# Optimization experiments

Measured on AMD Instinct MI355X. Metric: run time of the kernel, lower is better.

The kernel has to match this reference:

```python
import jax, jax.numpy as jnp
import numpy as np

B, C, IN, OUT = 2048, 64, 512, 512


def setup_inputs() -> dict:
    key = jax.random.key(0)
    k1, k2, k3 = jax.random.split(key, 3)
    x = jax.random.normal(k1, (B, IN), dtype=jnp.float32)
    index = jax.random.randint(k2, (B,), 0, C, dtype=jnp.int64)
    # kaiming_uniform-ish init: bound = sqrt(6 / ((1 + 5) * fan_in)) = 1/sqrt(fan_in)
    bound = 1.0 / np.sqrt(IN)
    weight = jax.random.uniform(k3, (C, OUT, IN), dtype=jnp.float32,
                                minval=-bound, maxval=bound)
    return {"input": x, "index": index, "weight": weight}


def reference(input, index, weight):
    # weight: (C, OUT, IN); index: (B,); input: (B, IN)
    w = weight[index]                      # (B, OUT, IN) gathered per-sample matrix
    return jnp.einsum('boi,bi->bo', w, input)  # batched matvec -> (B, OUT)
```

## Files before the change

### kernel.cpp

```cpp
#include <hip/hip_runtime.h>


constexpr int Bsz  = 2048;
constexpr int Ccnt = 64;
constexpr int INF  = 512;
constexpr int OUTF = 512;
constexpr int THREADS = 256;
constexpr int OT  = 16;
constexpr int TPB = 4;
constexpr int NBLK = Ccnt * (OUTF / (OT * TPB));

typedef __attribute__((ext_vector_type(8))) short bf16x8;
typedef __attribute__((ext_vector_type(4))) float f32x4;

#if __has_builtin(__builtin_amdgcn_cvt_pk_bf16_f32)
typedef __attribute__((ext_vector_type(2))) __bf16 bf16x2_t;
__device__ __forceinline__ int cvt2i(float a, float b) {
    union { bf16x2_t v; int i; } u;
    u.v = __builtin_amdgcn_cvt_pk_bf16_f32(a, b);
    return u.i;
}
#else
__device__ __forceinline__ unsigned f2bf(float f) {
    union { float f; unsigned u; } v; v.f = f;
    return (v.u + 0x7FFFu + ((v.u >> 16) & 1u)) >> 16;
}
__device__ __forceinline__ int cvt2i(float a, float b) {
    return (int)(f2bf(a) | (f2bf(b) << 16));
}
#endif

__device__ __forceinline__ bf16x8 cvt8(float4 a, float4 b) {
    union { bf16x8 v; int i[4]; } u;
    u.i[0] = cvt2i(a.x, a.y);
    u.i[1] = cvt2i(a.z, a.w);
    u.i[2] = cvt2i(b.x, b.y);
    u.i[3] = cvt2i(b.z, b.w);
    return u.v;
}

__device__ __forceinline__ void gld_lds16(const float* g, float* l) {
    __builtin_amdgcn_global_load_lds(
        (const __attribute__((address_space(1))) float*)g,
        (__attribute__((address_space(3))) float*)l, 16, 0, 0);
}

__device__ __forceinline__ void barrier_lgkm() {
    asm volatile("s_waitcnt lgkmcnt(0)" ::: "memory");
    __builtin_amdgcn_s_barrier();
    asm volatile("" ::: "memory");
}

__device__ __forceinline__ void stage_tile(const float* wt, float* dst,
                                           int wave, int lane) {
#pragma unroll
    for (int i = 0; i < 8; ++i) {
        const int inst = wave * 8 + i;
        const int r = inst >> 1;
        const int h = inst & 1;
        const int p = r & 7;
        const float* src = wt + (size_t)r * INF + (h * 64 + (lane ^ p)) * 4;
        gld_lds16(src, dst + inst * 256);
    }
}

__global__ __launch_bounds__(THREADS, 2)
void switching_linear_kernel(const float* __restrict__ x,
                             const int* __restrict__ idx,
                             const float* __restrict__ w,
                             float* __restrict__ out) {
    __shared__ float Wl[2][OT * INF];
    __shared__ unsigned short list[Bsz];
    __shared__ int ls_n;
    __shared__ float red[2][3][4][64];

    const int tid  = threadIdx.x;
    const int wave = tid >> 6;
    const int lane = tid & 63;

    const int bid   = ((int)blockIdx.x & 7) * (NBLK / 8) + ((int)blockIdx.x >> 3);
    const int c     = bid >> 3;
    const int obase = (bid & 7) * (OT * TPB);

    if (tid == 0) ls_n = 0;
    __syncthreads();

    const float* wc = w + (size_t)c * OUTF * INF + (size_t)obase * INF;

    stage_tile(wc, Wl[0], wave, lane);

    int my[8];
#pragma unroll
    for (int i = 0; i < 8; ++i) my[i] = idx[tid + i * THREADS];
#pragma unroll
    for (int i = 0; i < 8; ++i)
        if (my[i] == c) list[atomicAdd(&ls_n, 1)] = (unsigned short)(tid + i * THREADS);

    const int mrow = lane & 15;
    const int quad = lane >> 4;
    const int k0   = wave * (INF / 4);
    const int p    = mrow & 7;

    int n = 0;

    for (int ot = 0; ot < TPB; ++ot) {
        __syncthreads();
        if (ot == 0) {
            n = ls_n;
            if (n == 0) return;
        }
        if (ot + 1 < TPB)
            stage_tile(wc + (size_t)((ot + 1) * OT) * INF, Wl[(ot + 1) & 1],
                       wave, lane);

        const float* Wb = Wl[ot & 1];
        const int o0 = obase + ot * OT;

        bf16x8 wf[4];
#pragma unroll
        for (int t = 0; t < 4; ++t) {
            const int gb = (k0 >> 2) + t * 8 + quad * 2;
            float4 a0 = *(const float4*)&Wb[mrow * INF + ((gb)     ^ p) * 4];
            float4 a1 = *(const float4*)&Wb[mrow * INF + ((gb + 1) ^ p) * 4];
            wf[t] = cvt8(a0, a1);
        }

        for (int s0 = 0; s0 < n; s0 += 64) {
            const int rem = n - s0;
            const int ng  = rem >= 64 ? 4 : (rem + 15) >> 4;

            f32x4 acc[4];
#pragma unroll
            for (int g = 0; g < 4; ++g) acc[g] = (f32x4){0.f, 0.f, 0.f, 0.f};

#pragma unroll
            for (int g = 0; g < 4; ++g) {
                if (g < ng) {
                    const int s  = s0 + g * 16 + mrow;
                    const int sc = s < n ? s : n - 1;
                    const float* bp = x + (size_t)list[sc] * INF + k0 + quad * 8;
#pragma unroll
                    for (int i = 0; i < 4; ++i) {
                        float4 b0 = *(const float4*)(bp + i * 32);
                        float4 b1 = *(const float4*)(bp + i * 32 + 4);
                        acc[g] = __builtin_amdgcn_mfma_f32_16x16x32_bf16(
                                     wf[i], cvt8(b0, b1), acc[g], 0, 0, 0);
                    }
                }
            }

#pragma unroll
            for (int r0 = 0; r0 < 4; r0 += 2) {
                if (r0 < ng) {
                    if (wave != 0) {
#pragma unroll
                        for (int g = 0; g < 2; ++g) {
                            if (r0 + g < ng) {
#pragma unroll
                                for (int j = 0; j < 4; ++j)
                                    red[g][wave - 1][j][lane] = acc[r0 + g][j];
                            }
                        }
                    }
                    barrier_lgkm();
                    if (wave == 0) {
#pragma unroll
                        for (int g = 0; g < 2; ++g) {
                            if (r0 + g < ng) {
                                const int s = s0 + (r0 + g) * 16 + mrow;
                                if (s < n) {
                                    f32x4 a = acc[r0 + g];
#pragma unroll
                                    for (int wv2 = 0; wv2 < 3; ++wv2)
#pragma unroll
                                        for (int j = 0; j < 4; ++j)
                                            a[j] += red[g][wv2][j][lane];
                                    float* dst = out + (size_t)list[s] * OUTF
                                                     + o0 + quad * 4;
                                    *(float4*)dst = make_float4(a[0], a[1],
                                                                a[2], a[3]);
                                }
                            }
                        }
                    }
                    barrier_lgkm();
                }
            }
        }
    }
}

extern "C" void kernel_launch(void* const* d_in, const int* in_sizes, int n_in,
                              void* d_out, int out_size, void* d_ws, size_t ws_size,
                              hipStream_t stream) {
    const float* x   = (const float*)d_in[0];
    const int*   idx = (const int*)d_in[1];
    const float* w   = (const float*)d_in[2];
    float* out = (float*)d_out;

    switching_linear_kernel<<<dim3(NBLK), dim3(THREADS), 0, stream>>>(x, idx, w, out);
}
```

Before: 116.1 us.

## Split samples across waves instead of K, drop cross-wave LDS reduction

Each wave now owns a 16-sample group and covers the full K=512 dimension, so the cross-wave LDS reduction and its barriers are removed. The gathered x rows are loaded once into registers, converted to bf16, and reused across all four output tiles. Weight tiles are prefetched two ahead with vmcnt-based waits. The cost is higher register pressure (a 32-float4 raw buffer plus 16 bf16x8 fragments). With n around 32 per class, some waves sit idle, and each wave now reads more LDS per MFMA.

Result: faster. 106.4 us (-8.3%).

```diff
diff --git a/kernel.cpp b/kernel.cpp
--- a/kernel.cpp
+++ b/kernel.cpp
@@ -8,6 +8,7 @@
 constexpr int THREADS = 256;
 constexpr int OT  = 16;
 constexpr int TPB = 4;
+constexpr int NBUF = 2;
 constexpr int NBLK = Ccnt * (OUTF / (OT * TPB));
 
 typedef __attribute__((ext_vector_type(8))) short bf16x8;
@@ -51,6 +52,19 @@
     asm volatile("" ::: "memory");
 }
 
+__device__ __forceinline__ void vm8_barrier() {
+    asm volatile("s_waitcnt vmcnt(8)" ::: "memory");
+    __builtin_amdgcn_sched_barrier(0);
+    __builtin_amdgcn_s_barrier();
+    asm volatile("" ::: "memory");
+}
+__device__ __forceinline__ void vm0_barrier() {
+    asm volatile("s_waitcnt vmcnt(0)" ::: "memory");
+    __builtin_amdgcn_sched_barrier(0);
+    __builtin_amdgcn_s_barrier();
+    asm volatile("" ::: "memory");
+}
+
 __device__ __forceinline__ void stage_tile(const float* wt, float* dst,
                                            int wave, int lane) {
 #pragma unroll
@@ -69,10 +83,9 @@
                              const int* __restrict__ idx,
                              const float* __restrict__ w,
                              float* __restrict__ out) {
-    __shared__ float Wl[2][OT * INF];
+    __shared__ float Wl[NBUF][OT * INF];
     __shared__ unsigned short list[Bsz];
     __shared__ int ls_n;
-    __shared__ float red[2][3][4][64];
 
     const int tid  = threadIdx.x;
     const int wave = tid >> 6;
@@ -85,10 +98,6 @@
     if (tid == 0) ls_n = 0;
     __syncthreads();
 
-    const float* wc = w + (size_t)c * OUTF * INF + (size_t)obase * INF;
-
-    stage_tile(wc, Wl[0], wave, lane);
-
     int my[8];
 #pragma unroll
     for (int i = 0; i < 8; ++i) my[i] = idx[tid + i * THREADS];
@@ -96,96 +105,97 @@
     for (int i = 0; i < 8; ++i)
         if (my[i] == c) list[atomicAdd(&ls_n, 1)] = (unsigned short)(tid + i * THREADS);
 
+    __syncthreads();
+    const int n = ls_n;
+    if (n == 0) return;
+
     const int mrow = lane & 15;
     const int quad = lane >> 4;
-    const int k0   = wave * (INF / 4);
     const int p    = mrow & 7;
-
-    int n = 0;
+    const float* wc = w + (size_t)c * OUTF * INF + (size_t)obase * INF;
+
+    const int ng0    = (n >= 64) ? 4 : ((n + 15) >> 4);
+    const bool active = (wave < ng0);
+    const int s_my   = wave * 16 + mrow;
+    const int sc     = s_my < n ? s_my : n - 1;
+
+    float4 raw[32];
+    if (active) {
+        const float* bp = x + (size_t)list[sc] * INF + quad * 8;
+#pragma unroll
+        for (int kk = 0; kk < 16; ++kk) {
+            raw[2 * kk]     = *(const float4*)(bp + kk * 32);
+            raw[2 * kk + 1] = *(const float4*)(bp + kk * 32 + 4);
+        }
+    }
+    __builtin_amdgcn_sched_barrier(0);
+
+    stage_tile(wc,                    Wl[0], wave, lane);
+    stage_tile(wc + (size_t)OT * INF, Wl[1], wave, lane);
+
+    asm volatile("s_waitcnt vmcnt(16)" ::: "memory");
+    __builtin_amdgcn_sched_barrier(0);
+
+    bf16x8 xf[16];
+    if (active) {
+#pragma unroll
+        for (int kk = 0; kk < 16; ++kk)
+            xf[kk] = cvt8(raw[2 * kk], raw[2 * kk + 1]);
+    }
+
+    vm8_barrier();
 
     for (int ot = 0; ot < TPB; ++ot) {
-        __syncthreads();
-        if (ot == 0) {
-            n = ls_n;
-            if (n == 0) return;
-        }
-        if (ot + 1 < TPB)
-            stage_tile(wc + (size_t)((ot + 1) * OT) * INF, Wl[(ot + 1) & 1],
-                       wave, lane);
-
         const float* Wb = Wl[ot & 1];
         const int o0 = obase + ot * OT;
 
-        bf16x8 wf[4];
-#pragma unroll
-        for (int t = 0; t < 4; ++t) {
-            const int gb = (k0 >> 2) + t * 8 + quad * 2;
-            float4 a0 = *(const float4*)&Wb[mrow * INF + ((gb)     ^ p) * 4];
-            float4 a1 = *(const float4*)&Wb[mrow * INF + ((gb + 1) ^ p) * 4];
-            wf[t] = cvt8(a0, a1);
-        }
-
-        for (int s0 = 0; s0 < n; s0 += 64) {
-            const int rem = n - s0;
-            const int ng  = rem >= 64 ? 4 : (rem + 15) >> 4;
-
-            f32x4 acc[4];
-#pragma unroll
-            for (int g = 0; g < 4; ++g) acc[g] = (f32x4){0.f, 0.f, 0.f, 0.f};
-
-#pragma unroll
-            for (int g = 0; g < 4; ++g) {
-                if (g < ng) {
-                    const int s  = s0 + g * 16 + mrow;
-                    const int sc = s < n ? s : n - 1;
-                    const float* bp = x + (size_t)list[sc] * INF + k0 + quad * 8;
-#pragma unroll
-                    for (int i = 0; i < 4; ++i) {
-                        float4 b0 = *(const float4*)(bp + i * 32);
-                        float4 b1 = *(const float4*)(bp + i * 32 + 4);
-                        acc[g] = __builtin_amdgcn_mfma_f32_16x16x32_bf16(
-                                     wf[i], cvt8(b0, b1), acc[g], 0, 0, 0);
-                    }
+        if (active) {
+            f32x4 acc = (f32x4){0.f, 0.f, 0.f, 0.f};
+#pragma unroll
+            for (int kk = 0; kk < 16; ++kk) {
+                const int gb = kk * 8 + quad * 2;
+                float4 a0 = *(const float4*)&Wb[mrow * INF + ((gb)     ^ p) * 4];
+                float4 a1 = *(const float4*)&Wb[mrow * INF + ((gb + 1) ^ p) * 4];
+                acc = __builtin_amdgcn_mfma_f32_16x16x32_bf16(
+                          cvt8(a0, a1), xf[kk], acc, 0, 0, 0);
+            }
+            if (s_my < n) {
+                float* dst = out + (size_t)list[s_my] * OUTF + o0 + quad * 4;
+                *(float4*)dst = make_float4(acc[0], acc[1], acc[2], acc[3]);
+            }
+        }
+
+        for (int s0 = 64; s0 < n; s0 += 64) {
+            if (s0 + wave * 16 < n) {
+                const int s2  = s0 + wave * 16 + mrow;
+                const int sc2 = s2 < n ? s2 : n - 1;
+                const float* bp2 = x + (size_t)list[sc2] * INF + quad * 8;
+                f32x4 acc = (f32x4){0.f, 0.f, 0.f, 0.f};
+#pragma unroll
+                for (int kk = 0; kk < 16; ++kk) {
+                    const int gb = kk * 8 + quad * 2;
+                    float4 a0 = *(const float4*)&Wb[mrow * INF + ((gb)     ^ p) * 4];
+                    float4 a1 = *(const float4*)&Wb[mrow * INF + ((gb + 1) ^ p) * 4];
+                    float4 b0 = *(const float4*)(bp2 + kk * 32);
+                    float4 b1 = *(const float4*)(bp2 + kk * 32 + 4);
+                    acc = __builtin_amdgcn_mfma_f32_16x16x32_bf16(
+                              cvt8(a0, a1), cvt8(b0, b1), acc, 0, 0, 0);
+                }
+                if (s2 < n) {
+                    float* dst = out + (size_t)list[s2] * OUTF + o0 + quad * 4;
+                    *(float4*)dst = make_float4(acc[0], acc[1], acc[2], acc[3]);
                 }
             }
-
-#pragma unroll
-            for (int r0 = 0; r0 < 4; r0 += 2) {
-                if (r0 < ng) {
-                    if (wave != 0) {
-#pragma unroll
-                        for (int g = 0; g < 2; ++g) {
-                            if (r0 + g < ng) {
-#pragma unroll
-                                for (int j = 0; j < 4; ++j)
-                                    red[g][wave - 1][j][lane] = acc[r0 + g][j];
-                            }
-                        }
-                    }
-                    barrier_lgkm();
-                    if (wave == 0) {
-#pragma unroll
-                        for (int g = 0; g < 2; ++g) {
-                            if (r0 + g < ng) {
-                                const int s = s0 + (r0 + g) * 16 + mrow;
-                                if (s < n) {
-                                    f32x4 a = acc[r0 + g];
-#pragma unroll
-                                    for (int wv2 = 0; wv2 < 3; ++wv2)
-#pragma unroll
-                                        for (int j = 0; j < 4; ++j)
-                                            a[j] += red[g][wv2][j][lane];
-                                    float* dst = out + (size_t)list[s] * OUTF
-                                                     + o0 + quad * 4;
-                                    *(float4*)dst = make_float4(a[0], a[1],
-                                                                a[2], a[3]);
-                                }
-                            }
-                        }
-                    }
-                    barrier_lgkm();
-                }
-            }
+        }
+
+        if (ot + 2 < TPB) {
+            barrier_lgkm();
+            stage_tile(wc + (size_t)((ot + 2) * OT) * INF, Wl[ot & 1],
+                       wave, lane);
+        }
+        if (ot + 1 < TPB) {
+            if (ot + 2 < TPB) vm8_barrier();
+            else              vm0_barrier();
         }
     }
 }
```
